# Performance work log

Hardware: AMD Instinct MI355X
Metric: run time of the kernel (lower is better)

The kernel has to match this reference:

```python
import jax, jax.numpy as jnp
import numpy as np

B, N, FDIM, L, DH = 32, 4096, 128, 50, 4
EPS_NORM = 1e-12   # torch F.normalize default eps
EPS_COS = 1e-8     # torch F.cosine_similarity default eps
W1, W2, W3 = 0.3, 0.5, 0.4


def _l2norm(v, axis=-1, keepdims=True):
    return jnp.sqrt(jnp.sum(v * v, axis=axis, keepdims=keepdims))


def _normalize(v):
    # F.normalize: v / max(||v||, eps)
    return v / jnp.maximum(_l2norm(v), EPS_NORM)


def _cosine_sim(a, b):
    # F.cosine_similarity along last dim with eps clamp on norms
    num = jnp.sum(a * b, axis=-1)
    den = jnp.maximum(_l2norm(a, keepdims=False), EPS_COS) * \
          jnp.maximum(_l2norm(b, keepdims=False), EPS_COS)
    return num / den


def setup_inputs() -> dict:
    key = jax.random.key(0)
    k1, k2, k3 = jax.random.split(key, 3)
    x_encoder_agents = jax.random.normal(k1, (B, N, FDIM), dtype=jnp.float32)
    hist_feat = jax.random.normal(k2, (B, N, L, DH), dtype=jnp.float32)
    hist_embed = jax.random.normal(k3, (B, N, FDIM), dtype=jnp.float32)
    return {"x_encoder_agents": x_encoder_agents,
            "hist_feat": hist_feat,
            "hist_embed": hist_embed,
            "k": 8}


def reference(x_encoder_agents, hist_feat, hist_embed, k):
    # x_encoder_agents: (B, N, F); hist_feat: (B, N, L, 4); hist_embed: (B, N, F)
    center_agent = x_encoder_agents[:, 0, :]          # (B, F)
    others = x_encoder_agents[:, 1:, :]               # (B, N-1, F)

    # distance score
    diff = others - center_agent[:, None, :]
    distances = _l2norm(diff, keepdims=False)         # (B, N-1)

    # velocity (heading) cosine similarity from last two history positions
    pos_diff = hist_feat[..., -2:, :2]                # (B, N, 2, 2)
    direction = pos_diff[..., 1, :] - pos_diff[..., 0, :]  # (B, N, 2)
    center_dir = _normalize(direction[:, 0, :]) + 1e-8      # (B, 2)
    others_dir = _normalize(direction[:, 1:, :]) + 1e-8     # (B, N-1, 2)
    velocity_sim = _cosine_sim(others_dir, center_dir[:, None, :])  # (B, N-1)

    # trajectory embedding cosine similarity
    center_emb = hist_embed[:, 0, :]
    others_emb = hist_embed[:, 1:, :]
    traj_sim = _cosine_sim(others_emb, center_emb[:, None, :])       # (B, N-1)

    score = (W1 * distances
             + W2 * (1.0 - jnp.maximum(velocity_sim, 0.0))
             + W3 * (1.0 - jnp.maximum(traj_sim, 0.0)))

    # topk smallest score (torch.topk largest=False)
    _, indices = jax.lax.top_k(-score, k)             # (B, k), ascending score

    closest_agents = jnp.take_along_axis(others, indices[..., None], axis=1)  # (B, k, F)
    return closest_agents, indices
```

## Files before the change

kernel.cpp:

```cpp
#include <hip/hip_runtime.h>

#define BATCH 32
#define NAG   4096
#define FDIM  128
#define LREC  200
#define KSEL  8

__global__ __launch_bounds__(256) void score_kernel(
    const float* __restrict__ x,
    const float* __restrict__ hf,
    const float* __restrict__ he,
    float* __restrict__ scores)
{
    const int gtid = blockIdx.x * 256 + threadIdx.x;
    const int wave = gtid >> 6;
    const int lane = threadIdx.x & 63;
    const int b = wave >> 12;
    const int n = wave & (NAG - 1);
    if (b >= BATCH) return;

    if (n == 0) {
        if (lane == 0) scores[(size_t)b * NAG] = 1e30f;
        return;
    }

    const size_t rown = (size_t)(b * NAG + n) * FDIM;
    const size_t rowc = (size_t)(b * NAG) * FDIM;

    const float2 a = ((const float2*)(x  + rown))[lane];
    const float2 c = ((const float2*)(x  + rowc))[lane];
    const float2 e = ((const float2*)(he + rown))[lane];
    const float2 f = ((const float2*)(he + rowc))[lane];

    const float dx = a.x - c.x, dy = a.y - c.y;
    float dist2 = dx * dx + dy * dy;
    float dotv  = e.x * f.x + e.y * f.y;
    float nn    = e.x * e.x + e.y * e.y;
    float cc    = f.x * f.x + f.y * f.y;

    #pragma unroll
    for (int m = 32; m; m >>= 1) {
        dist2 += __shfl_xor(dist2, m, 64);
        dotv  += __shfl_xor(dotv,  m, 64);
        nn    += __shfl_xor(nn,    m, 64);
        cc    += __shfl_xor(cc,    m, 64);
    }

    if (lane == 0) {
        const float dist = sqrtf(dist2);
        const float traj = dotv / (fmaxf(sqrtf(nn), 1e-8f) * fmaxf(sqrtf(cc), 1e-8f));

        const float* hn = hf + (size_t)(b * NAG + n) * LREC + 192;
        const float* h0 = hf + (size_t)(b * NAG)     * LREC + 192;
        const float dnx = hn[4] - hn[0], dny = hn[5] - hn[1];
        const float d0x = h0[4] - h0[0], d0y = h0[5] - h0[1];

        const float n0  = fmaxf(sqrtf(d0x * d0x + d0y * d0y), 1e-12f);
        const float cdx = d0x / n0 + 1e-8f, cdy = d0y / n0 + 1e-8f;
        const float nn2 = fmaxf(sqrtf(dnx * dnx + dny * dny), 1e-12f);
        const float odx = dnx / nn2 + 1e-8f, ody = dny / nn2 + 1e-8f;

        const float num = odx * cdx + ody * cdy;
        const float den = fmaxf(sqrtf(odx * odx + ody * ody), 1e-8f) *
                          fmaxf(sqrtf(cdx * cdx + cdy * cdy), 1e-8f);
        const float vel = num / den;

        const float score = 0.3f * dist
                          + 0.5f * (1.0f - fmaxf(vel,  0.0f))
                          + 0.4f * (1.0f - fmaxf(traj, 0.0f));
        scores[(size_t)b * NAG + n] = score;
    }
}

__global__ __launch_bounds__(256) void topk_gather_kernel(
    const float* __restrict__ scores,
    const float* __restrict__ x,
    float* __restrict__ out)
{
    const int b   = blockIdx.x;
    const int tid = threadIdx.x;

    __shared__ float s[NAG];
    __shared__ int   sel[KSEL];
    __shared__ float red_s[4];
    __shared__ int   red_i[4];

    for (int i = tid; i < NAG; i += 256)
        s[i] = scores[(size_t)b * NAG + i];
    __syncthreads();

    for (int r = 0; r < KSEL; ++r) {
        float best = 1e30f;
        int   bi   = 0x7fffffff;
        for (int i = tid; i < NAG; i += 256) {
            const float v = s[i];
            if (v < best || (v == best && i < bi)) { best = v; bi = i; }
        }
        #pragma unroll
        for (int m = 32; m; m >>= 1) {
            const float ov = __shfl_xor(best, m, 64);
            const int   oi = __shfl_xor(bi,   m, 64);
            if (ov < best || (ov == best && oi < bi)) { best = ov; bi = oi; }
        }
        if ((tid & 63) == 0) { red_s[tid >> 6] = best; red_i[tid >> 6] = bi; }
        __syncthreads();
        if (tid == 0) {
            float bb = red_s[0]; int ii = red_i[0];
            #pragma unroll
            for (int w = 1; w < 4; ++w)
                if (red_s[w] < bb || (red_s[w] == bb && red_i[w] < ii)) {
                    bb = red_s[w]; ii = red_i[w];
                }
            sel[r] = ii;
            s[ii] = 1e30f;
        }
        __syncthreads();
    }

    for (int e2 = tid; e2 < KSEL * FDIM; e2 += 256) {
        const int j = e2 >> 7;
        const int d = e2 & 127;
        const int n = sel[j];
        out[((size_t)b * KSEL + j) * FDIM + d] = x[(size_t)(b * NAG + n) * FDIM + d];
    }
    if (tid < KSEL)
        out[(size_t)BATCH * KSEL * FDIM + b * KSEL + tid] = (float)(sel[tid] - 1);
}

extern "C" void kernel_launch(void* const* d_in, const int* in_sizes, int n_in,
                              void* d_out, int out_size, void* d_ws, size_t ws_size,
                              hipStream_t stream) {
    const float* x  = (const float*)d_in[0];
    const float* hf = (const float*)d_in[1];
    const float* he = (const float*)d_in[2];
    float* out = (float*)d_out;
    float* scores = (float*)d_ws;

    const int total_waves  = BATCH * NAG;
    const int blocks1      = total_waves / 4;
    score_kernel<<<blocks1, 256, 0, stream>>>(x, hf, he, scores);

    topk_gather_kernel<<<BATCH, 256, 0, stream>>>(scores, x, out);
}
```

Before: 252.7 us.

## Process two agents per wave with float4 loads and register-resident top-k

```diff
diff --git a/kernel.cpp b/kernel.cpp
--- a/kernel.cpp
+++ b/kernel.cpp
@@ -15,45 +15,47 @@
     const int gtid = blockIdx.x * 256 + threadIdx.x;
     const int wave = gtid >> 6;
     const int lane = threadIdx.x & 63;
-    const int b = wave >> 12;
-    const int n = wave & (NAG - 1);
-    if (b >= BATCH) return;
+    const int half = lane >> 5;
+    const int sub  = lane & 31;
 
-    if (n == 0) {
-        if (lane == 0) scores[(size_t)b * NAG] = 1e30f;
-        return;
-    }
+    const int b = wave >> 11;
+    const int p = wave & 2047;
+    const int n = 2 * p + half;
 
-    const size_t rown = (size_t)(b * NAG + n) * FDIM;
-    const size_t rowc = (size_t)(b * NAG) * FDIM;
+    const size_t rown = ((size_t)(b << 12) + n) * FDIM;
+    const size_t rowc = ((size_t)(b << 12)) * FDIM;
 
-    const float2 a = ((const float2*)(x  + rown))[lane];
-    const float2 c = ((const float2*)(x  + rowc))[lane];
-    const float2 e = ((const float2*)(he + rown))[lane];
-    const float2 f = ((const float2*)(he + rowc))[lane];
+    const float4 a = *(const float4*)(x  + rown + sub * 4);
+    const float4 c = *(const float4*)(x  + rowc + sub * 4);
+    const float4 e = *(const float4*)(he + rown + sub * 4);
+    const float4 f = *(const float4*)(he + rowc + sub * 4);
 
-    const float dx = a.x - c.x, dy = a.y - c.y;
-    float dist2 = dx * dx + dy * dy;
-    float dotv  = e.x * f.x + e.y * f.y;
-    float nn    = e.x * e.x + e.y * e.y;
-    float cc    = f.x * f.x + f.y * f.y;
+    const float dx0 = a.x - c.x, dx1 = a.y - c.y, dx2 = a.z - c.z, dx3 = a.w - c.w;
+    float dist2 = dx0 * dx0 + dx1 * dx1 + dx2 * dx2 + dx3 * dx3;
+    float dotv  = e.x * f.x + e.y * f.y + e.z * f.z + e.w * f.w;
+    float nn    = e.x * e.x + e.y * e.y + e.z * e.z + e.w * e.w;
+    float cc    = f.x * f.x + f.y * f.y + f.z * f.z + f.w * f.w;
 
     #pragma unroll
-    for (int m = 32; m; m >>= 1) {
+    for (int m = 16; m; m >>= 1) {
         dist2 += __shfl_xor(dist2, m, 64);
         dotv  += __shfl_xor(dotv,  m, 64);
         nn    += __shfl_xor(nn,    m, 64);
         cc    += __shfl_xor(cc,    m, 64);
     }
 
-    if (lane == 0) {
+    if (sub == 0) {
         const float dist = sqrtf(dist2);
         const float traj = dotv / (fmaxf(sqrtf(nn), 1e-8f) * fmaxf(sqrtf(cc), 1e-8f));
 
-        const float* hn = hf + (size_t)(b * NAG + n) * LREC + 192;
-        const float* h0 = hf + (size_t)(b * NAG)     * LREC + 192;
-        const float dnx = hn[4] - hn[0], dny = hn[5] - hn[1];
-        const float d0x = h0[4] - h0[0], d0y = h0[5] - h0[1];
+        const float* hn = hf + ((size_t)(b << 12) + n) * LREC + 192;
+        const float* h0 = hf + ((size_t)(b << 12)) * LREC + 192;
+        const float2 hn0 = *(const float2*)(hn);
+        const float2 hn1 = *(const float2*)(hn + 4);
+        const float2 h00 = *(const float2*)(h0);
+        const float2 h01 = *(const float2*)(h0 + 4);
+        const float dnx = hn1.x - hn0.x, dny = hn1.y - hn0.y;
+        const float d0x = h01.x - h00.x, d0y = h01.y - h00.y;
 
         const float n0  = fmaxf(sqrtf(d0x * d0x + d0y * d0y), 1e-12f);
         const float cdx = d0x / n0 + 1e-8f, cdy = d0y / n0 + 1e-8f;
@@ -68,7 +70,7 @@
         const float score = 0.3f * dist
                           + 0.5f * (1.0f - fmaxf(vel,  0.0f))
                           + 0.4f * (1.0f - fmaxf(traj, 0.0f));
-        scores[(size_t)b * NAG + n] = score;
+        scores[(size_t)(b << 12) + n] = (n == 0) ? 1e30f : score;
     }
 }
 
@@ -80,21 +82,23 @@
     const int b   = blockIdx.x;
     const int tid = threadIdx.x;
 
-    __shared__ float s[NAG];
-    __shared__ int   sel[KSEL];
+    float v[16];
+    #pragma unroll
+    for (int j = 0; j < 16; ++j)
+        v[j] = scores[(size_t)(b << 12) + (j << 8) + tid];
+
     __shared__ float red_s[4];
     __shared__ int   red_i[4];
-
-    for (int i = tid; i < NAG; i += 256)
-        s[i] = scores[(size_t)b * NAG + i];
-    __syncthreads();
+    __shared__ int   sel[KSEL];
 
     for (int r = 0; r < KSEL; ++r) {
         float best = 1e30f;
         int   bi   = 0x7fffffff;
-        for (int i = tid; i < NAG; i += 256) {
-            const float v = s[i];
-            if (v < best || (v == best && i < bi)) { best = v; bi = i; }
+        #pragma unroll
+        for (int j = 0; j < 16; ++j) {
+            const int   i  = (j << 8) + tid;
+            const float vv = v[j];
+            if (vv < best || (vv == best && i < bi)) { best = vv; bi = i; }
         }
         #pragma unroll
         for (int m = 32; m; m >>= 1) {
@@ -112,16 +116,17 @@
                     bb = red_s[w]; ii = red_i[w];
                 }
             sel[r] = ii;
-            s[ii] = 1e30f;
         }
         __syncthreads();
+        const int w = sel[r];
+        if ((w & 255) == tid) v[w >> 8] = 1e30f;
     }
 
     for (int e2 = tid; e2 < KSEL * FDIM; e2 += 256) {
         const int j = e2 >> 7;
         const int d = e2 & 127;
         const int n = sel[j];
-        out[((size_t)b * KSEL + j) * FDIM + d] = x[(size_t)(b * NAG + n) * FDIM + d];
+        out[((size_t)b * KSEL + j) * FDIM + d] = x[((size_t)(b << 12) + n) * FDIM + d];
     }
     if (tid < KSEL)
         out[(size_t)BATCH * KSEL * FDIM + b * KSEL + tid] = (float)(sel[tid] - 1);
@@ -136,8 +141,7 @@
     float* out = (float*)d_out;
     float* scores = (float*)d_ws;
 
-    const int total_waves  = BATCH * NAG;
-    const int blocks1      = total_waves / 4;
+    const int blocks1 = (BATCH * (NAG / 2) * 64) / 256;
     score_kernel<<<blocks1, 256, 0, stream>>>(x, hf, he, scores);
 
     topk_gather_kernel<<<BATCH, 256, 0, stream>>>(scores, x, out);
```

Result: faster. 234.6 us (-7.2%).
